# Optimization experiments

Hardware: AMD Instinct MI355X
Metric: run time of the kernel (lower is better)

Reference implementation:

```python
import jax, jax.numpy as jnp
import numpy as np

HOP = 32  # stride from init_kwargs


def setup_inputs() -> dict:
    key = jax.random.key(0)
    kc, kv = jax.random.split(key)
    B, N, K, L = 8, 512, 32768, 64
    c = jax.random.normal(kc, (B, N, K), dtype=jnp.float32)
    V = jax.random.normal(kv, (L, N), dtype=jnp.float32) * 0.01
    return {"c": c, "V": V}


def reference(c, V):
    # c: [B, N, K], V: [L, N]
    B, N, K = c.shape
    L = V.shape[0]
    T_out = (K - 1) * HOP + L
    # all per-frame projections in one batched GEMM: [B, K, L]
    frames = jnp.einsum('ln,bnk->bkl', V, c)
    # overlap-add: frame k writes to samples [k*HOP, k*HOP+L)
    idx = (jnp.arange(K)[:, None] * HOP + jnp.arange(L)[None, :]).reshape(-1)  # [K*L]
    y = jnp.zeros((B, T_out), dtype=c.dtype).at[:, idx].add(frames.reshape(B, K * L))
    return y[:, None, :]  # [B, 1, T_out]
```

## Files before the change

### kernel.cpp

```cpp
#include <hip/hip_runtime.h>
#include <hip/hip_bf16.h>

#define HOP 32
#define NB 8
#define NDIM 512
#define KDIM 32768
#define LDIM 64
#define TOUT ((KDIM - 1) * HOP + LDIM)
#define QTILE 64
#define CT_ROWS 72
#define CT_STRIDE 520

typedef __bf16 bf16x8 __attribute__((ext_vector_type(8)));
typedef float floatx4 __attribute__((ext_vector_type(4)));

__device__ __forceinline__ unsigned short f2bf(float f) {
    unsigned int u = __float_as_uint(f);
    u += 0x7FFFu + ((u >> 16) & 1u);
    return (unsigned short)(u >> 16);
}

__global__ void convert_v_kernel(const float* __restrict__ vf,
                                 unsigned short* __restrict__ vb) {
    int i = (blockIdx.x * 256 + threadIdx.x) * 4;
    float4 v = *reinterpret_cast<const float4*>(vf + i);
    ushort4 o;
    o.x = f2bf(v.x); o.y = f2bf(v.y); o.z = f2bf(v.z); o.w = f2bf(v.w);
    *reinterpret_cast<ushort4*>(vb + i) = o;
}

__global__ __launch_bounds__(256, 2) void decoder_kernel(
        const float* __restrict__ cg,
        const unsigned short* __restrict__ vb,
        float* __restrict__ outg)
{
    __shared__ __align__(16) unsigned short ct[CT_ROWS * CT_STRIDE];

    const int tid  = threadIdx.x;
    const int tile = blockIdx.x;
    const int b    = blockIdx.y;
    const int q0   = tile * QTILE;
    const int lane = tid & 63;

    const long cbase = (long)b * NDIM * KDIM;

    const bool fastA = (q0 + QTILE <= KDIM);
    #pragma unroll 4
    for (int it = 0; it < 32; ++it) {
        int id = it * 256 + tid;
        int n  = id >> 4;
        int cc = id & 15;
        int colbase = q0 + cc * 4;
        float4 v;
        if (fastA) {
            v = *reinterpret_cast<const float4*>(cg + cbase + (long)n * KDIM + colbase);
        } else {
            float* ve = reinterpret_cast<float*>(&v);
            #pragma unroll
            for (int e = 0; e < 4; ++e) {
                int col = colbase + e;
                ve[e] = (col < KDIM) ? cg[cbase + (long)n * KDIM + col] : 0.f;
            }
        }
        unsigned short s[4];
        s[0] = f2bf(v.x); s[1] = f2bf(v.y); s[2] = f2bf(v.z); s[3] = f2bf(v.w);
        #pragma unroll
        for (int i = 0; i < 4; ++i) {
            int e = (lane + i) & 3;
            ct[(8 + cc * 4 + e) * CT_STRIDE + n] = s[e];
        }
    }
    const bool fastB = (q0 >= 8);
    #pragma unroll
    for (int it = 0; it < 4; ++it) {
        int id = it * 256 + tid;
        int n  = id >> 1;
        int cc = id & 1;
        int colbase = q0 - 8 + cc * 4;
        float4 v;
        if (fastB) {
            v = *reinterpret_cast<const float4*>(cg + cbase + (long)n * KDIM + colbase);
        } else {
            float* ve = reinterpret_cast<float*>(&v);
            #pragma unroll
            for (int e = 0; e < 4; ++e) {
                int col = colbase + e;
                ve[e] = (col >= 0) ? cg[cbase + (long)n * KDIM + col] : 0.f;
            }
        }
        unsigned short s[4];
        s[0] = f2bf(v.x); s[1] = f2bf(v.y); s[2] = f2bf(v.z); s[3] = f2bf(v.w);
        #pragma unroll
        for (int i = 0; i < 4; ++i) {
            int e = (lane + i) & 3;
            ct[(cc * 4 + e) * CT_STRIDE + n] = s[e];
        }
    }
    __syncthreads();

    const int w   = tid >> 6;
    const int l15 = lane & 15;
    const int g   = lane >> 4;

    floatx4 acc0 = {0.f, 0.f, 0.f, 0.f};
    floatx4 acc1 = {0.f, 0.f, 0.f, 0.f};

    const int jlo = w * 16 + l15;

    #pragma unroll 4
    for (int ks = 0; ks < 32; ++ks) {
        const int hi   = (ks >= 16);
        const int ncol = (ks & 15) * 32 + g * 8;
        const unsigned short* bp = &ct[(jlo + (hi ? 7 : 8)) * CT_STRIDE + ncol];
        bf16x8 bfrag = *reinterpret_cast<const bf16x8*>(bp);
        const int vrow0 = l15 + (hi ? 32 : 0);
        bf16x8 a0 = *reinterpret_cast<const bf16x8*>(vb + vrow0 * NDIM + ncol);
        bf16x8 a1 = *reinterpret_cast<const bf16x8*>(vb + (vrow0 + 16) * NDIM + ncol);
        acc0 = __builtin_amdgcn_mfma_f32_16x16x32_bf16(a0, bfrag, acc0, 0, 0, 0);
        acc1 = __builtin_amdgcn_mfma_f32_16x16x32_bf16(a1, bfrag, acc1, 0, 0, 0);
    }

    const int q = q0 + w * 16 + l15;
    if (q <= KDIM) {
        long tb = (long)b * TOUT + (long)q * HOP + g * 4;
        *reinterpret_cast<floatx4*>(outg + tb)      = acc0;
        *reinterpret_cast<floatx4*>(outg + tb + 16) = acc1;
    }
}

extern "C" void kernel_launch(void* const* d_in, const int* in_sizes, int n_in,
                              void* d_out, int out_size, void* d_ws, size_t ws_size,
                              hipStream_t stream) {
    const float* c  = (const float*)d_in[0];
    const float* V  = (const float*)d_in[1];
    float* out      = (float*)d_out;
    unsigned short* vb = (unsigned short*)d_ws;

    convert_v_kernel<<<dim3(32), dim3(256), 0, stream>>>(V, vb);
    dim3 grid(KDIM / QTILE + 1, NB);
    decoder_kernel<<<grid, dim3(256, 1, 1), 0, stream>>>(c, vb, out);
}
```

Before: 847.7 us.

## Double-buffer the N dimension in LDS and raise occupancy to four blocks

The shared-memory tile for c is now split along N into four chunks of 128 and held in two buffers. Loading and converting the next chunk overlaps with the MFMA work on the current one. Shared memory per block drops from about 75KB to about 39KB, which allows launch bounds of four blocks per CU instead of two. The risks are extra barriers, more register pressure from the unrolled stage loads, and possible spills under the tighter launch bound.

```diff
diff --git a/kernel.cpp b/kernel.cpp
--- a/kernel.cpp
+++ b/kernel.cpp
@@ -9,7 +9,8 @@
 #define TOUT ((KDIM - 1) * HOP + LDIM)
 #define QTILE 64
 #define CT_ROWS 72
-#define CT_STRIDE 520
+#define NSPLIT 128
+#define CT_STRIDE 136
 
 typedef __bf16 bf16x8 __attribute__((ext_vector_type(8)));
 typedef float floatx4 __attribute__((ext_vector_type(4)));
@@ -29,12 +30,12 @@
     *reinterpret_cast<ushort4*>(vb + i) = o;
 }
 
-__global__ __launch_bounds__(256, 2) void decoder_kernel(
+__global__ __launch_bounds__(256, 4) void decoder_kernel(
         const float* __restrict__ cg,
         const unsigned short* __restrict__ vb,
         float* __restrict__ outg)
 {
-    __shared__ __align__(16) unsigned short ct[CT_ROWS * CT_STRIDE];
+    __shared__ __align__(16) unsigned short ct[2][CT_ROWS * CT_STRIDE];
 
     const int tid  = threadIdx.x;
     const int tile = blockIdx.x;
@@ -43,81 +44,90 @@
     const int lane = tid & 63;
 
     const long cbase = (long)b * NDIM * KDIM;
-
     const bool fastA = (q0 + QTILE <= KDIM);
-    #pragma unroll 4
-    for (int it = 0; it < 32; ++it) {
-        int id = it * 256 + tid;
-        int n  = id >> 4;
-        int cc = id & 15;
-        int colbase = q0 + cc * 4;
-        float4 v;
-        if (fastA) {
-            v = *reinterpret_cast<const float4*>(cg + cbase + (long)n * KDIM + colbase);
-        } else {
-            float* ve = reinterpret_cast<float*>(&v);
-            #pragma unroll
-            for (int e = 0; e < 4; ++e) {
-                int col = colbase + e;
-                ve[e] = (col < KDIM) ? cg[cbase + (long)n * KDIM + col] : 0.f;
-            }
-        }
-        unsigned short s[4];
-        s[0] = f2bf(v.x); s[1] = f2bf(v.y); s[2] = f2bf(v.z); s[3] = f2bf(v.w);
-        #pragma unroll
-        for (int i = 0; i < 4; ++i) {
-            int e = (lane + i) & 3;
-            ct[(8 + cc * 4 + e) * CT_STRIDE + n] = s[e];
-        }
-    }
     const bool fastB = (q0 >= 8);
-    #pragma unroll
-    for (int it = 0; it < 4; ++it) {
-        int id = it * 256 + tid;
-        int n  = id >> 1;
-        int cc = id & 1;
-        int colbase = q0 - 8 + cc * 4;
-        float4 v;
-        if (fastB) {
-            v = *reinterpret_cast<const float4*>(cg + cbase + (long)n * KDIM + colbase);
-        } else {
-            float* ve = reinterpret_cast<float*>(&v);
-            #pragma unroll
-            for (int e = 0; e < 4; ++e) {
-                int col = colbase + e;
-                ve[e] = (col >= 0) ? cg[cbase + (long)n * KDIM + col] : 0.f;
-            }
-        }
-        unsigned short s[4];
-        s[0] = f2bf(v.x); s[1] = f2bf(v.y); s[2] = f2bf(v.z); s[3] = f2bf(v.w);
-        #pragma unroll
-        for (int i = 0; i < 4; ++i) {
-            int e = (lane + i) & 3;
-            ct[(cc * 4 + e) * CT_STRIDE + n] = s[e];
-        }
-    }
-    __syncthreads();
 
     const int w   = tid >> 6;
     const int l15 = lane & 15;
     const int g   = lane >> 4;
+    const int jlo = w * 16 + l15;
 
     floatx4 acc0 = {0.f, 0.f, 0.f, 0.f};
     floatx4 acc1 = {0.f, 0.f, 0.f, 0.f};
 
-    const int jlo = w * 16 + l15;
+    auto stage = [&](int n0, int s) {
+        #pragma unroll
+        for (int it = 0; it < 8; ++it) {
+            int id = it * 256 + tid;
+            int n  = id >> 4;
+            int cc = id & 15;
+            int colbase = q0 + cc * 4;
+            float4 v;
+            if (fastA) {
+                v = *reinterpret_cast<const float4*>(cg + cbase + (long)(n0 + n) * KDIM + colbase);
+            } else {
+                float* ve = reinterpret_cast<float*>(&v);
+                #pragma unroll
+                for (int e = 0; e < 4; ++e) {
+                    int col = colbase + e;
+                    ve[e] = (col < KDIM) ? cg[cbase + (long)(n0 + n) * KDIM + col] : 0.f;
+                }
+            }
+            unsigned short sr[4];
+            sr[0] = f2bf(v.x); sr[1] = f2bf(v.y); sr[2] = f2bf(v.z); sr[3] = f2bf(v.w);
+            #pragma unroll
+            for (int i = 0; i < 4; ++i) {
+                int e = (lane + i) & 3;
+                ct[s][(8 + cc * 4 + e) * CT_STRIDE + n] = sr[e];
+            }
+        }
+        {
+            int n  = tid >> 1;
+            int cc = tid & 1;
+            int colbase = q0 - 8 + cc * 4;
+            float4 v;
+            if (fastB) {
+                v = *reinterpret_cast<const float4*>(cg + cbase + (long)(n0 + n) * KDIM + colbase);
+            } else {
+                float* ve = reinterpret_cast<float*>(&v);
+                #pragma unroll
+                for (int e = 0; e < 4; ++e) {
+                    int col = colbase + e;
+                    ve[e] = (col >= 0) ? cg[cbase + (long)(n0 + n) * KDIM + col] : 0.f;
+                }
+            }
+            unsigned short sr[4];
+            sr[0] = f2bf(v.x); sr[1] = f2bf(v.y); sr[2] = f2bf(v.z); sr[3] = f2bf(v.w);
+            #pragma unroll
+            for (int i = 0; i < 4; ++i) {
+                int e = (lane + i) & 3;
+                ct[s][(cc * 4 + e) * CT_STRIDE + n] = sr[e];
+            }
+        }
+    };
 
-    #pragma unroll 4
-    for (int ks = 0; ks < 32; ++ks) {
-        const int hi   = (ks >= 16);
-        const int ncol = (ks & 15) * 32 + g * 8;
-        const unsigned short* bp = &ct[(jlo + (hi ? 7 : 8)) * CT_STRIDE + ncol];
-        bf16x8 bfrag = *reinterpret_cast<const bf16x8*>(bp);
-        const int vrow0 = l15 + (hi ? 32 : 0);
-        bf16x8 a0 = *reinterpret_cast<const bf16x8*>(vb + vrow0 * NDIM + ncol);
-        bf16x8 a1 = *reinterpret_cast<const bf16x8*>(vb + (vrow0 + 16) * NDIM + ncol);
-        acc0 = __builtin_amdgcn_mfma_f32_16x16x32_bf16(a0, bfrag, acc0, 0, 0, 0);
-        acc1 = __builtin_amdgcn_mfma_f32_16x16x32_bf16(a1, bfrag, acc1, 0, 0, 0);
+    auto mma = [&](int n0, int s) {
+        #pragma unroll
+        for (int ks = 0; ks < 8; ++ks) {
+            const int hi   = (ks >= 4);
+            const int ncol = (ks & 3) * 32 + g * 8;
+            const unsigned short* bp = &ct[s][(jlo + (hi ? 7 : 8)) * CT_STRIDE + ncol];
+            bf16x8 bfrag = *reinterpret_cast<const bf16x8*>(bp);
+            const int vrow0 = l15 + (hi ? 32 : 0);
+            bf16x8 a0 = *reinterpret_cast<const bf16x8*>(vb + vrow0 * NDIM + n0 + ncol);
+            bf16x8 a1 = *reinterpret_cast<const bf16x8*>(vb + (vrow0 + 16) * NDIM + n0 + ncol);
+            acc0 = __builtin_amdgcn_mfma_f32_16x16x32_bf16(a0, bfrag, acc0, 0, 0, 0);
+            acc1 = __builtin_amdgcn_mfma_f32_16x16x32_bf16(a1, bfrag, acc1, 0, 0, 0);
+        }
+    };
+
+    stage(0, 0);
+    __syncthreads();
+    #pragma unroll
+    for (int p = 0; p < 4; ++p) {
+        if (p < 3) stage((p + 1) * NSPLIT, (p + 1) & 1);
+        mma(p * NSPLIT, p & 1);
+        __syncthreads();
     }
 
     const int q = q0 + w * 16 + l15;
```

Result: faster. 795.3 us (-6.2%).
